# Optimization experiments

Measured on AMD Instinct MI355X. Metric: run time of the kernel, lower is better.

The kernel has to match this reference:

```python
import jax, jax.numpy as jnp
import numpy as np

BS, SL, N_AGENTS, OBS_DIM, STATE_DIM, N_EDGES, HID = 32, 512, 32, 96, 1024, 64, 256


def _hgcn(w_line, x, H):
    # x: [B, n, 1]; H: [B, n, E]. Faithful to torch HGCN:
    # A = D^{-1/2} H |W| B^{-1} H^T D^{-1/2}, with D, B built from detached H/|W|,
    # inf entries (from 0^{-1} / 0^{-0.5}) zeroed. Diagonal matmuls are implicit scalings.
    w_abs = jnp.abs(w_line)
    Hd = jax.lax.stop_gradient(H)
    d = jnp.einsum('bne,e->bn', Hd, jax.lax.stop_gradient(w_abs))  # [B, n]
    d_is = jnp.where(d > 0, jax.lax.rsqrt(jnp.where(d > 0, d, 1.0)), 0.0)
    b = jnp.sum(Hd, axis=-2)  # [B, E]
    b_inv = jnp.where(b > 0, 1.0 / jnp.where(b > 0, b, 1.0), 0.0)
    t = d_is[..., None] * x                       # D^{-1/2} x
    s = jnp.einsum('bne,bnk->bek', H, t)          # H^T (...)
    s = s * (w_abs[None, :] * b_inv)[..., None]   # |W| B^{-1} (diagonals commute)
    y = jnp.einsum('bne,bek->bnk', H, s)          # H (...)
    return d_is[..., None] * y                    # D^{-1/2} (...)


def _mlp(x, w1, b1, w2, b2):
    return jax.nn.relu(x @ w1 + b1) @ w2 + b2


def setup_inputs() -> dict:
    key = jax.random.key(0)
    ks = jax.random.split(key, 24)
    f = jax.random.normal
    inp = {
        'agent_qs': f(ks[0], (BS, SL, N_AGENTS), jnp.float32),
        'states': f(ks[1], (BS, SL, STATE_DIM), jnp.float32),
        'indiv_us': f(ks[2], (BS, SL, N_AGENTS, OBS_DIM), jnp.float32),
        'edge_W': f(ks[3], (OBS_DIM, N_EDGES), jnp.float32) * 0.1,
        'edge_b': f(ks[4], (N_EDGES,), jnp.float32) * 0.1,
        'wline1': 1.0 + 0.1 * f(ks[5], (N_EDGES,), jnp.float32),
        'wline2': 1.0 + 0.1 * f(ks[6], (N_EDGES,), jnp.float32),
    }
    names = ['hw1', 'hc1', 'hw', 'hc']
    outs = [N_AGENTS, N_AGENTS, N_AGENTS, 1]
    for i, (nm, od) in enumerate(zip(names, outs)):
        inp[nm + '_w1'] = f(ks[7 + 4 * i], (STATE_DIM, HID), jnp.float32) * 0.05
        inp[nm + '_b1'] = f(ks[8 + 4 * i], (HID,), jnp.float32) * 0.05
        inp[nm + '_w2'] = f(ks[9 + 4 * i], (HID, od), jnp.float32) * 0.05
        inp[nm + '_b2'] = f(ks[10 + 4 * i], (od,), jnp.float32) * 0.05
    return inp


def reference(agent_qs, states, indiv_us, edge_W, edge_b, wline1, wline2,
              hw1_w1, hw1_b1, hw1_w2, hw1_b2, hc1_w1, hc1_b1, hc1_w2, hc1_b2,
              hw_w1, hw_b1, hw_w2, hw_b2, hc_w1, hc_b1, hc_w2, hc_b2):
    bs, sl, n = agent_qs.shape
    q = agent_qs.reshape(-1, n)                               # [B, n]
    u = indiv_us.reshape(-1, n, indiv_us.shape[-1])           # [B, n, obs]
    s = states.reshape(-1, states.shape[-1])                  # [B, state_dim]
    H = jax.nn.relu(u @ edge_W + edge_b)                      # hyper_edge_net -> [B, n, E]
    x = q[..., None]                                          # node_features [B, n, 1]
    qs_tot = _hgcn(wline2, _hgcn(wline1, x, H), H)[..., 0]    # two stacked HGCN encoders
    w1 = jnp.abs(_mlp(s, hw1_w1, hw1_b1, hw1_w2, hw1_b2))
    c1 = _mlp(s, hc1_w1, hc1_b1, hc1_w2, hc1_b2)
    qt = jax.nn.elu(qs_tot * w1 + c1)
    w = jnp.abs(_mlp(s, hw_w1, hw_b1, hw_w2, hw_b2))
    c = _mlp(s, hc_w1, hc_b1, hc_w2, hc_b2)[..., 0]
    q_tot = jnp.sum(qt * w, axis=-1) + c
    return q_tot.reshape(bs, sl, 1)
```

## Files before the change

kernel.cpp:

```cpp
#include <hip/hip_runtime.h>
#include <cstdint>

typedef _Float16 f16;
typedef _Float16 f16x2 __attribute__((ext_vector_type(2)));
typedef _Float16 f16x4 __attribute__((ext_vector_type(4)));
typedef _Float16 f16x8 __attribute__((ext_vector_type(8)));
typedef float f32x4 __attribute__((ext_vector_type(4)));

#define AS1U const __attribute__((address_space(1))) unsigned int
#define AS3U __attribute__((address_space(3))) unsigned int

__device__ __forceinline__ void gload_lds16(const void* g, void* l) {
    __builtin_amdgcn_global_load_lds((AS1U*)g, (AS3U*)l, 16, 0, 0);
}

#define WSYNC() asm volatile("s_waitcnt lgkmcnt(0)" ::: "memory")

#define BATCH 16384
#define NAG   32
#define OBS   96
#define SDIM  1024
#define NE    64
#define HIDN  256
#define NH    1024

#define NB_ST 1024
#define NB_PW 256
#define NB_SM 101
#define NB_FRONT (NB_ST + NB_PW + NB_SM)

__global__ __launch_bounds__(256) void k_front(
    const float* __restrict__ states,
    const float* __restrict__ w1a, const float* __restrict__ w1b,
    const float* __restrict__ w1c, const float* __restrict__ w1d,
    const float* __restrict__ b1a, const float* __restrict__ b1b,
    const float* __restrict__ b1c, const float* __restrict__ b1d,
    const float* __restrict__ w2a, const float* __restrict__ w2b,
    const float* __restrict__ w2c, const float* __restrict__ w2d,
    f16* __restrict__ states16, f16* __restrict__ W1t, float* __restrict__ b1cat,
    f16* __restrict__ W2t, f16* __restrict__ hcw2) {
    __shared__ float tile[64 * 65];
    const int tid = threadIdx.x;
    int bid = blockIdx.x;

    if (bid < NB_ST) {
        int i = bid * 256 + tid;
        const int n4 = BATCH * SDIM / 4;
        const int stride = NB_ST * 256;
        for (; i < n4; i += stride) {
            float4 v = ((const float4*)states)[i];
            f16x4 h = { (f16)v.x, (f16)v.y, (f16)v.z, (f16)v.w };
            ((f16x4*)states16)[i] = h;
        }
        return;
    }
    bid -= NB_ST;
    if (bid < NB_PW) {
        int mlp = bid >> 6, rem = bid & 63, kt = rem >> 2, ct = rem & 3;
        const float* src = (mlp == 0) ? w1a : (mlp == 1) ? w1b : (mlp == 2) ? w1c : w1d;
        int k0 = kt * 64, c0 = ct * 64;
        for (int i = tid; i < 4096; i += 256) {
            int kk = i >> 6, cc = i & 63;
            tile[kk * 65 + cc] = src[(size_t)(k0 + kk) * 256 + c0 + cc];
        }
        __syncthreads();
        for (int i = tid; i < 4096; i += 256) {
            int cc = i >> 6, kk = i & 63;
            W1t[(size_t)(mlp * 256 + c0 + cc) * 1024 + k0 + kk] = (f16)tile[kk * 65 + cc];
        }
        return;
    }
    bid -= NB_PW;
    {
        int i = bid * 256 + tid;
        if (i < 24576) {
            int mp = i >> 13, rem = i & 8191, oo = rem >> 8, kk = rem & 255;
            const float* src = (mp == 0) ? w2a : (mp == 1) ? w2b : w2c;
            W2t[i] = (f16)src[kk * 32 + oo];
        } else if (i < 24832) {
            int k = i - 24576;
            hcw2[k] = (f16)w2d[k];
        } else if (i < 25856) {
            int n = i - 24832;
            int mlp = n >> 8, c = n & 255;
            const float* bsrc = (mlp == 0) ? b1a : (mlp == 1) ? b1b : (mlp == 2) ? b1c : b1d;
            b1cat[n] = bsrc[c];
        }
    }
}

__global__ __launch_bounds__(512) void k_gemm(
    const f16* __restrict__ A, const f16* __restrict__ B,
    const float* __restrict__ b1cat, const f16* __restrict__ W2t,
    const f16* __restrict__ hcw2, float* __restrict__ Pp) {
    __shared__ __align__(16) char smem[131072];
    f16* Asb = (f16*)smem;
    f16* Bsb = (f16*)(smem + 65536);
    f16* Ts  = (f16*)smem;

    const int tid = threadIdx.x;
    const int w = tid >> 6, l = tid & 63;
    const int lm = l & 15, lk = l >> 4;
    const int wm = w >> 2, wn = w & 3;
    const int p = blockIdx.x;
    const int xcd = p & 7, s = p >> 3;
    const int mt = xcd * 8 + (s >> 2);
    const int nt = s & 3;
    const int m0 = mt * 256, n0 = nt * 256;
    const int c0 = w * 4;
    const int srow = l >> 3, scol = (l & 7) * 8;

    f32x4 acc[8][4];
    #pragma unroll
    for (int i = 0; i < 8; i++)
        #pragma unroll
        for (int j = 0; j < 4; j++) acc[i][j] = (f32x4){0.f, 0.f, 0.f, 0.f};

    #pragma unroll
    for (int i = 0; i < 4; i++) {
        int cc = c0 + i;
        gload_lds16(&A[(size_t)(m0 + cc * 8 + srow) * 1024 + scol], &Asb[cc * 512]);
        gload_lds16(&B[(size_t)(n0 + cc * 8 + srow) * 1024 + scol], &Bsb[cc * 512]);
    }
    __syncthreads();

    int cur = 0;
    for (int kt = 0; kt < 16; kt++) {
        if (kt < 15) {
            f16* Ad = Asb + (cur ^ 1) * 16384;
            f16* Bd = Bsb + (cur ^ 1) * 16384;
            #pragma unroll
            for (int i = 0; i < 4; i++) {
                int cc = c0 + i;
                gload_lds16(&A[(size_t)(m0 + cc * 8 + srow) * 1024 + (kt + 1) * 64 + scol], &Ad[cc * 512]);
                gload_lds16(&B[(size_t)(n0 + cc * 8 + srow) * 1024 + (kt + 1) * 64 + scol], &Bd[cc * 512]);
            }
        }
        const f16* As_ = Asb + cur * 16384;
        const f16* Bs_ = Bsb + cur * 16384;
        #pragma unroll
        for (int ks = 0; ks < 2; ks++) {
            f16x8 af[8], bf[4];
            #pragma unroll
            for (int i = 0; i < 8; i++)
                af[i] = *(const f16x8*)&As_[(wm * 128 + i * 16 + lm) * 64 + ks * 32 + lk * 8];
            #pragma unroll
            for (int j = 0; j < 4; j++)
                bf[j] = *(const f16x8*)&Bs_[(wn * 64 + j * 16 + lm) * 64 + ks * 32 + lk * 8];
            #pragma unroll
            for (int i = 0; i < 8; i++)
                #pragma unroll
                for (int j = 0; j < 4; j++)
                    acc[i][j] = __builtin_amdgcn_mfma_f32_16x16x32_f16(af[i], bf[j], acc[i][j], 0, 0, 0);
        }
        __syncthreads();
        cur ^= 1;
    }

    float bj[4];
    #pragma unroll
    for (int j = 0; j < 4; j++) bj[j] = b1cat[n0 + wn * 64 + j * 16 + lm];
    const int mlp = nt;

    #pragma unroll
    for (int pass = 0; pass < 2; pass++) {
        if (wm == pass) {
            #pragma unroll
            for (int i = 0; i < 8; i++)
                #pragma unroll
                for (int r = 0; r < 4; r++) {
                    int rl = i * 16 + lk * 4 + r;
                    #pragma unroll
                    for (int j = 0; j < 4; j++) {
                        float v = acc[i][j][r] + bj[j];
                        Ts[rl * 264 + wn * 64 + j * 16 + lm] = (f16)(v > 0.f ? v : 0.f);
                    }
                }
        }
        __syncthreads();
        const int grow = m0 + pass * 128 + w * 16;
        if (mlp < 3) {
            const f16* wb = W2t + mlp * 8192;
            f32x4 acc2[2];
            acc2[0] = (f32x4){0, 0, 0, 0}; acc2[1] = (f32x4){0, 0, 0, 0};
            #pragma unroll
            for (int ks = 0; ks < 8; ks++) {
                f16x8 a  = *(const f16x8*)&Ts[(w * 16 + lm) * 264 + ks * 32 + lk * 8];
                f16x8 b0 = *(const f16x8*)&wb[lm * 256 + ks * 32 + lk * 8];
                f16x8 b1 = *(const f16x8*)&wb[(16 + lm) * 256 + ks * 32 + lk * 8];
                acc2[0] = __builtin_amdgcn_mfma_f32_16x16x32_f16(a, b0, acc2[0], 0, 0, 0);
                acc2[1] = __builtin_amdgcn_mfma_f32_16x16x32_f16(a, b1, acc2[1], 0, 0, 0);
            }
            #pragma unroll
            for (int j2 = 0; j2 < 2; j2++)
                #pragma unroll
                for (int r = 0; r < 4; r++)
                    Pp[(size_t)(grow + lk * 4 + r) * 104 + mlp * 32 + j2 * 16 + lm] = acc2[j2][r];
        } else {
            f32x4 acc2 = (f32x4){0, 0, 0, 0};
            #pragma unroll
            for (int ks = 0; ks < 8; ks++) {
                f16x8 a = *(const f16x8*)&Ts[(w * 16 + lm) * 264 + ks * 32 + lk * 8];
                f16x8 bz = (f16x8){0, 0, 0, 0, 0, 0, 0, 0};
                if (lm == 0) bz = *(const f16x8*)&hcw2[ks * 32 + lk * 8];
                acc2 = __builtin_amdgcn_mfma_f32_16x16x32_f16(a, bz, acc2, 0, 0, 0);
            }
            if (lm == 0)
                #pragma unroll
                for (int r = 0; r < 4; r++)
                    Pp[(size_t)(grow + lk * 4 + r) * 104 + 96] = acc2[r];
        }
        if (pass == 0) __syncthreads();
    }
}

__global__ __launch_bounds__(256) void k_hgcn_ep(
    const float* __restrict__ agent_qs, const float* __restrict__ indiv_us,
    const float* __restrict__ edge_W, const float* __restrict__ edge_b,
    const float* __restrict__ wline1, const float* __restrict__ wline2,
    const float* __restrict__ Pp,
    const float* __restrict__ hw1_b2, const float* __restrict__ hc1_b2,
    const float* __restrict__ hw_b2, const float* __restrict__ hc_b2,
    float* __restrict__ out) {
    __shared__ __align__(16) char arena[34304];
    f16*   eWs   = (f16*)arena;
    float* swa   = (float*)(arena + 13312);
    f16*   HsB   = (f16*)(arena + 13824);
    float* svB   = (float*)(arena + 30720);
    float* sttB  = (float*)(arena + 31744);
    float* sdisB = (float*)(arena + 32256);
    float* sbinvB= (float*)(arena + 33280);

    const int tid = threadIdx.x;
    const int w = tid >> 6, l = tid & 63;
    const int b = blockIdx.x * 4 + w;
    f16*   Hw    = HsB + w * (32 * 66);
    float* sv    = svB + w * 64;
    float* stt   = sttB + w * 32;
    float* sdis  = sdisB + w * 64;
    float* sbinv = sbinvB + w * 64;

    const int nn = l & 31, half = l >> 5;

    float pa0 = 0.f, pc0 = 0.f, pw0 = 0.f;
    float p96a = 0.f, bw1 = 0.f, bc1 = 0.f, bww = 0.f, bhc = 0.f;
    if (half == 0) {
        const float* p0 = Pp + (size_t)b * 104;
        pa0 = p0[nn];
        pc0 = p0[32 + nn];
        pw0 = p0[64 + nn];
        p96a = p0[96];
        bw1 = hw1_b2[nn];  bc1 = hc1_b2[nn];
        bww = hw_b2[nn];   bhc = hc_b2[0];
    }
    float q = agent_qs[(size_t)b * 32 + nn];

    for (int i = tid; i < 6144; i += 256) {
        int k = i >> 6, n = i & 63;
        eWs[n * 104 + k] = (f16)edge_W[i];
    }
    if (tid < 64) swa[tid] = fabsf(wline1[tid]);
    else if (tid < 128) swa[tid] = fabsf(wline2[tid - 64]);
    __syncthreads();

    const int lm = l & 15, lk = l >> 4;
    const float* ub = indiv_us + (size_t)b * (NAG * OBS);

    #pragma unroll
    for (int mt = 0; mt < 2; mt++) {
        f16x8 af[3];
        #pragma unroll
        for (int ks = 0; ks < 3; ks++) {
            const float* up = ub + (mt * 16 + lm) * 96 + ks * 32 + lk * 8;
            float4 v0 = *(const float4*)up;
            float4 v1 = *(const float4*)(up + 4);
            af[ks] = (f16x8){ (f16)v0.x, (f16)v0.y, (f16)v0.z, (f16)v0.w,
                              (f16)v1.x, (f16)v1.y, (f16)v1.z, (f16)v1.w };
        }
        #pragma unroll
        for (int nt = 0; nt < 4; nt++) {
            f32x4 acc = {0.f, 0.f, 0.f, 0.f};
            #pragma unroll
            for (int ks = 0; ks < 3; ks++) {
                f16x8 bb = *(const f16x8*)&eWs[(nt * 16 + lm) * 104 + ks * 32 + lk * 8];
                acc = __builtin_amdgcn_mfma_f32_16x16x32_f16(af[ks], bb, acc, 0, 0, 0);
            }
            int col = nt * 16 + lm;
            float bias = edge_b[col];
            #pragma unroll
            for (int r = 0; r < 4; r++) {
                int row = mt * 16 + lk * 4 + r;
                float hv = acc[r] + bias;
                Hw[row * 66 + col] = (f16)(hv > 0.f ? hv : 0.f);
            }
        }
    }
    WSYNC();

    float bsum = 0.f;
    #pragma unroll
    for (int n = 0; n < 32; n++) bsum += (float)Hw[n * 66 + l];
    sbinv[l] = bsum > 0.f ? 1.f / bsum : 0.f;

    float dd = 0.f;
    #pragma unroll 8
    for (int e2 = 0; e2 < 32; e2++) {
        f16x2 h2 = *(const f16x2*)&Hw[nn * 66 + e2 * 2];
        dd += (float)h2.x * swa[half * 64 + e2 * 2] + (float)h2.y * swa[half * 64 + e2 * 2 + 1];
    }
    float dis = dd > 0.f ? rsqrtf(dd) : 0.f;
    sdis[l] = dis;
    if (half == 0) stt[nn] = dis * q;
    WSYNC();

    float s1 = 0.f;
    #pragma unroll
    for (int n = 0; n < 32; n++) s1 += (float)Hw[n * 66 + l] * stt[n];
    sv[l] = s1 * swa[l] * sbinv[l];
    WSYNC();

    float y1 = 0.f;
    #pragma unroll 8
    for (int e2 = 0; e2 < 32; e2++) {
        f16x2 h2 = *(const f16x2*)&Hw[nn * 66 + e2 * 2];
        y1 += (float)h2.x * sv[e2 * 2] + (float)h2.y * sv[e2 * 2 + 1];
    }
    float x2 = sdis[nn] * y1;
    if (half == 0) stt[nn] = sdis[32 + nn] * x2;
    WSYNC();

    float s2 = 0.f;
    #pragma unroll
    for (int n = 0; n < 32; n++) s2 += (float)Hw[n * 66 + l] * stt[n];
    sv[l] = s2 * swa[64 + l] * sbinv[l];
    WSYNC();

    float y2 = 0.f;
    #pragma unroll 8
    for (int e2 = 0; e2 < 32; e2++) {
        f16x2 h2 = *(const f16x2*)&Hw[nn * 66 + e2 * 2];
        y2 += (float)h2.x * sv[e2 * 2] + (float)h2.y * sv[e2 * 2 + 1];
    }

    float qsv = sdis[32 + nn] * y2;
    float w1v = fabsf(pa0 + bw1);
    float c1v = pc0 + bc1;
    float wwv = fabsf(pw0 + bww);
    float z = qsv * w1v + c1v;
    float qt = z > 0.f ? z : expm1f(z);
    float val = (half == 0) ? qt * wwv : 0.f;
    val += __shfl_xor(val, 1, 32);
    val += __shfl_xor(val, 2, 32);
    val += __shfl_xor(val, 4, 32);
    val += __shfl_xor(val, 8, 32);
    val += __shfl_xor(val, 16, 32);
    if (l == 0) out[b] = val + p96a + bhc;
}

extern "C" void kernel_launch(void* const* d_in, const int* in_sizes, int n_in,
                              void* d_out, int out_size, void* d_ws, size_t ws_size,
                              hipStream_t stream) {
    const float* agent_qs = (const float*)d_in[0];
    const float* states   = (const float*)d_in[1];
    const float* indiv_us = (const float*)d_in[2];
    const float* edge_W   = (const float*)d_in[3];
    const float* edge_b   = (const float*)d_in[4];
    const float* wline1   = (const float*)d_in[5];
    const float* wline2   = (const float*)d_in[6];
    const float* hw1_w1 = (const float*)d_in[7];
    const float* hw1_b1 = (const float*)d_in[8];
    const float* hw1_w2 = (const float*)d_in[9];
    const float* hw1_b2 = (const float*)d_in[10];
    const float* hc1_w1 = (const float*)d_in[11];
    const float* hc1_b1 = (const float*)d_in[12];
    const float* hc1_w2 = (const float*)d_in[13];
    const float* hc1_b2 = (const float*)d_in[14];
    const float* hw_w1  = (const float*)d_in[15];
    const float* hw_b1  = (const float*)d_in[16];
    const float* hw_w2  = (const float*)d_in[17];
    const float* hw_b2  = (const float*)d_in[18];
    const float* hc_w1  = (const float*)d_in[19];
    const float* hc_b1  = (const float*)d_in[20];
    const float* hc_w2  = (const float*)d_in[21];
    const float* hc_b2  = (const float*)d_in[22];

    char* ws = (char*)d_ws;
    size_t o_states16 = 0;
    size_t o_W1t  = o_states16 + (size_t)BATCH * SDIM * 2;
    size_t o_b1   = o_W1t + (size_t)NH * SDIM * 2;
    size_t o_W2t  = o_b1 + 4096;
    size_t o_hcw2 = o_W2t + 49152;
    size_t o_Pp   = o_hcw2 + 512;

    f16*   states16 = (f16*)(ws + o_states16);
    f16*   W1t      = (f16*)(ws + o_W1t);
    float* b1cat    = (float*)(ws + o_b1);
    f16*   W2t      = (f16*)(ws + o_W2t);
    f16*   hcw2     = (f16*)(ws + o_hcw2);
    float* Pp       = (float*)(ws + o_Pp);

    k_front<<<NB_FRONT, 256, 0, stream>>>(
        states,
        hw1_w1, hc1_w1, hw_w1, hc_w1, hw1_b1, hc1_b1, hw_b1, hc_b1,
        hw1_w2, hc1_w2, hw_w2, hc_w2,
        states16, W1t, b1cat, W2t, hcw2);
    k_gemm<<<256, 512, 0, stream>>>(states16, W1t, b1cat, W2t, hcw2, Pp);
    k_hgcn_ep<<<BATCH / 4, 256, 0, stream>>>(
        agent_qs, indiv_us, edge_W, edge_b, wline1, wline2, Pp,
        hw1_b2, hc1_b2, hw_b2, hc_b2, (float*)d_out);
}
```

Before: 124.1 us.

## Prefetch two K-tiles ahead with vmcnt waits and XOR-swizzled LDS layout

Restructures the GEMM main loop so two K-tiles are issued up front, and each iteration waits with a partial vmcnt count instead of a full syncthreads. This lets the next tile's global-to-LDS loads overlap the current tile's MFMA work. It also XOR-swizzles the 16-byte chunk placement in LDS to cut bank conflicts on fragment reads, and raises wave priority around the MFMA block. The vmcnt accounting relies on exact load counts per wave, so any miscount would cause races.

```diff
diff --git a/kernel.cpp b/kernel.cpp
--- a/kernel.cpp
+++ b/kernel.cpp
@@ -15,6 +15,7 @@
 }
 
 #define WSYNC() asm volatile("s_waitcnt lgkmcnt(0)" ::: "memory")
+#define CFENCE() asm volatile("" ::: "memory")
 
 #define BATCH 16384
 #define NAG   32
@@ -108,7 +109,12 @@
     const int nt = s & 3;
     const int m0 = mt * 256, n0 = nt * 256;
     const int c0 = w * 4;
-    const int srow = l >> 3, scol = (l & 7) * 8;
+    const int srow = l >> 3;
+    const int gchunk = (l & 7) ^ srow;
+
+    float bj[4];
+    #pragma unroll
+    for (int j = 0; j < 4; j++) bj[j] = b1cat[n0 + wn * 64 + j * 16 + lm];
 
     f32x4 acc[8][4];
     #pragma unroll
@@ -116,52 +122,55 @@
         #pragma unroll
         for (int j = 0; j < 4; j++) acc[i][j] = (f32x4){0.f, 0.f, 0.f, 0.f};
 
-    #pragma unroll
-    for (int i = 0; i < 4; i++) {
-        int cc = c0 + i;
-        gload_lds16(&A[(size_t)(m0 + cc * 8 + srow) * 1024 + scol], &Asb[cc * 512]);
-        gload_lds16(&B[(size_t)(n0 + cc * 8 + srow) * 1024 + scol], &Bsb[cc * 512]);
-    }
-    __syncthreads();
-
-    int cur = 0;
+#define STAGE(KT, BI)                                                                     \
+    {                                                                                     \
+        f16* Ad = Asb + (BI) * 16384;                                                     \
+        f16* Bd = Bsb + (BI) * 16384;                                                     \
+        _Pragma("unroll")                                                                 \
+        for (int i_ = 0; i_ < 4; i_++) {                                                  \
+            int cc = c0 + i_;                                                             \
+            gload_lds16(&A[(size_t)(m0 + cc * 8 + srow) * 1024 + (KT) * 64 + gchunk * 8], \
+                        &Ad[cc * 512]);                                                   \
+            gload_lds16(&B[(size_t)(n0 + cc * 8 + srow) * 1024 + (KT) * 64 + gchunk * 8], \
+                        &Bd[cc * 512]);                                                   \
+        }                                                                                 \
+    }
+
+    STAGE(0, 0);
+    STAGE(1, 1);
+
     for (int kt = 0; kt < 16; kt++) {
-        if (kt < 15) {
-            f16* Ad = Asb + (cur ^ 1) * 16384;
-            f16* Bd = Bsb + (cur ^ 1) * 16384;
-            #pragma unroll
-            for (int i = 0; i < 4; i++) {
-                int cc = c0 + i;
-                gload_lds16(&A[(size_t)(m0 + cc * 8 + srow) * 1024 + (kt + 1) * 64 + scol], &Ad[cc * 512]);
-                gload_lds16(&B[(size_t)(n0 + cc * 8 + srow) * 1024 + (kt + 1) * 64 + scol], &Bd[cc * 512]);
-            }
-        }
-        const f16* As_ = Asb + cur * 16384;
-        const f16* Bs_ = Bsb + cur * 16384;
+        if (kt < 15) { asm volatile("s_waitcnt vmcnt(8)" ::: "memory"); }
+        else         { asm volatile("s_waitcnt vmcnt(0)" ::: "memory"); }
+        CFENCE(); __builtin_amdgcn_s_barrier(); CFENCE();
+
+        const f16* As_ = Asb + (kt & 1) * 16384;
+        const f16* Bs_ = Bsb + (kt & 1) * 16384;
+        __builtin_amdgcn_s_setprio(1);
         #pragma unroll
         for (int ks = 0; ks < 2; ks++) {
+            const int sw = (((ks * 4 + lk) ^ (lm & 7)) << 3);
             f16x8 af[8], bf[4];
             #pragma unroll
             for (int i = 0; i < 8; i++)
-                af[i] = *(const f16x8*)&As_[(wm * 128 + i * 16 + lm) * 64 + ks * 32 + lk * 8];
+                af[i] = *(const f16x8*)&As_[(wm * 128 + i * 16 + lm) * 64 + sw];
             #pragma unroll
             for (int j = 0; j < 4; j++)
-                bf[j] = *(const f16x8*)&Bs_[(wn * 64 + j * 16 + lm) * 64 + ks * 32 + lk * 8];
+                bf[j] = *(const f16x8*)&Bs_[(wn * 64 + j * 16 + lm) * 64 + sw];
             #pragma unroll
             for (int i = 0; i < 8; i++)
                 #pragma unroll
                 for (int j = 0; j < 4; j++)
                     acc[i][j] = __builtin_amdgcn_mfma_f32_16x16x32_f16(af[i], bf[j], acc[i][j], 0, 0, 0);
         }
-        __syncthreads();
-        cur ^= 1;
-    }
-
-    float bj[4];
-    #pragma unroll
-    for (int j = 0; j < 4; j++) bj[j] = b1cat[n0 + wn * 64 + j * 16 + lm];
+        __builtin_amdgcn_s_setprio(0);
+
+        CFENCE(); __builtin_amdgcn_s_barrier(); CFENCE();
+        if (kt < 14) STAGE(kt + 2, kt & 1);
+    }
+#undef STAGE
+
     const int mlp = nt;
-
     #pragma unroll
     for (int pass = 0; pass < 2; pass++) {
         if (wm == pass) {
```

Result: faster. 120.6 us (-2.8%).
